# Kernel tuning notes

Measured on AMD Instinct MI355X. Metric: run time of the kernel, lower is better.

The kernel has to match this reference:

```python
import jax, jax.numpy as jnp
import numpy as np

B, N, DIM, H, DH = 8, 1024, 512, 8, 64
INNER = H * DH
SCALE = DH ** -0.5


def setup_inputs() -> dict:
    key = jax.random.key(0)
    ks = jax.random.split(key, 9)
    s = 0.02
    return {
        "x": jax.random.normal(ks[0], (B, N, DIM), jnp.float32),
        "lidar": jax.random.normal(ks[1], (B, N, INNER), jnp.float32),
        "w_qkv": jax.random.normal(ks[2], (3 * INNER, DIM), jnp.float32) * s,
        "w_merge": jax.random.normal(ks[3], (DH, DH), jnp.float32) * s,
        "b_merge": jnp.zeros((DH,), jnp.float32),
        "w_out": jax.random.normal(ks[4], (DIM, INNER), jnp.float32) * s,
        "b_out": jnp.zeros((DIM,), jnp.float32),
        "conv_w": jax.random.normal(ks[5], (2,), jnp.float32) * 0.5,
        "conv_b": jnp.zeros((), jnp.float32),
    }


def _split_heads(t):  # [b, n, h*d] -> [b, h, n, d]
    b, n, _ = t.shape
    return t.reshape(b, n, H, DH).transpose(0, 2, 1, 3)


def reference(x, lidar, w_qkv, w_merge, b_merge, w_out, b_out, conv_w, conv_b):
    b, n, _ = x.shape
    qkv = x @ w_qkv.T  # [b, n, 3*inner]
    q, k, v = jnp.split(qkv, 3, axis=-1)
    q, k, v = _split_heads(q), _split_heads(k), _split_heads(v)
    lid = _split_heads(lidar)

    dots = jnp.einsum('bhid,bhjd->bhij', q, k) * SCALE
    lidar_sim = jnp.einsum('bhid,bhjd->bhij', lid, lid) * SCALE
    lidar_sim = jax.nn.softmax(lidar_sim, axis=-1)

    # 1x1 conv over 2 channels == learned linear blend of the two score maps
    mid = conv_w[0] * dots + conv_w[1] * lidar_sim + conv_b
    attn = jax.nn.softmax(mid, axis=-1)

    out = jnp.einsum('bhij,bhjd->bhid', attn, v)
    out = out @ w_merge.T + b_merge                  # per-head linear_merge
    out = out.transpose(0, 2, 1, 3).reshape(b, n, INNER)  # b h n d -> b n (h d)
    out = out @ w_out.T + b_out                      # to_out (dropout = identity)
    return (out, lidar)
```

## Files before the change

kernel.cpp:

```cpp
#include <hip/hip_runtime.h>
#include <hip/hip_bf16.h>

#define B_      8
#define N_      1024
#define DIM_    512
#define H_      8
#define DH_     64
#define INNER_  512
#define SCALE_  0.125f
#define LOG2E_  1.4426950408889634f

typedef __attribute__((ext_vector_type(8))) __bf16         bf16x8;
typedef __attribute__((ext_vector_type(8))) unsigned short ushort8;
typedef __attribute__((ext_vector_type(4))) float          f32x4;

union FragCast { ushort8 u; bf16x8 b; };
union FragU32  { unsigned int u[4]; bf16x8 b; };

__device__ inline bf16x8 ld_frag(const unsigned short* p) {
    FragCast f; f.u = *(const ushort8*)p; return f.b;
}

__device__ inline f32x4 mfma16(bf16x8 a, bf16x8 b, f32x4 c) {
    return __builtin_amdgcn_mfma_f32_16x16x32_bf16(a, b, c, 0, 0, 0);
}

__device__ inline float fexp2(float x) { return __builtin_amdgcn_exp2f(x); }

__device__ inline unsigned short f2bf(float x) {
    unsigned int u = __float_as_uint(x);
    unsigned int lsb = (u >> 16) & 1u;
    u += 0x7fffu + lsb;
    return (unsigned short)(u >> 16);
}

__device__ inline unsigned int pack_bf2(float hi, float lo) {
    return __builtin_amdgcn_perm(__float_as_uint(hi), __float_as_uint(lo), 0x07060302u);
}

__device__ inline void gl_lds(const unsigned short* g, unsigned short* l) {
    __builtin_amdgcn_global_load_lds(
        (const __attribute__((address_space(1))) unsigned int*)g,
        (__attribute__((address_space(3))) unsigned int*)l, 16, 0, 0);
}

__global__ __launch_bounds__(256) void k_convert(
    const float* __restrict__ x, const float* __restrict__ lidar,
    const float* __restrict__ wqkv, const float* __restrict__ wmerge,
    const float* __restrict__ wout,
    unsigned short* __restrict__ x_bf, unsigned short* __restrict__ lid_bf,
    float* __restrict__ out_lidar,
    unsigned short* __restrict__ wqkv_bf, unsigned short* __restrict__ wm_bf,
    unsigned short* __restrict__ wout_bf)
{
    const int bx = blockIdx.x, tid = threadIdx.x;
    const float* src; unsigned short* dst; bool isLid = false; long base;
    if (bx < 1024)      { src = x;      dst = x_bf;    base = (long)bx * 1024; }
    else if (bx < 2048) { src = lidar;  dst = lid_bf;  base = (long)(bx - 1024) * 1024; isLid = true; }
    else if (bx < 2240) { src = wqkv;   dst = wqkv_bf; base = (long)(bx - 2048) * 1024; }
    else if (bx < 2304) { src = wout;   dst = wout_bf; base = (long)(bx - 2240) * 1024; }
    else                { src = wmerge; dst = wm_bf;   base = 0; }
    for (int k = 0; k < 4; k++) {
        long j = base + k * 256 + tid;
        float4 v = ((const float4*)src)[j];
        ushort4 o;
        o.x = f2bf(v.x); o.y = f2bf(v.y); o.z = f2bf(v.z); o.w = f2bf(v.w);
        ((ushort4*)dst)[j] = o;
        if (isLid) ((float4*)out_lidar)[j] = v;
    }
}

__global__ __launch_bounds__(256) void k_gemm_qkv(
    const unsigned short* __restrict__ A, const unsigned short* __restrict__ Bm,
    unsigned short* __restrict__ C, unsigned short* __restrict__ vt,
    int M, int Nd, int K)
{
    __shared__ unsigned short sMem[128 * 136];
    unsigned short* sA = sMem;
    unsigned short* sB = sMem + 128 * 64;
    const int tid  = threadIdx.x;
    const int lane = tid & 63, wave = tid >> 6;
    const int q = lane >> 4, l15 = lane & 15, l7 = l15 & 7;
    const int xq0 = (q ^ l7) << 3, xq4 = ((q + 4) ^ l7) << 3;
    const int m0 = blockIdx.x * 128, n0 = blockIdx.y * 128;
    const int wm = (wave >> 1) * 64, wn = (wave & 1) * 64;
    f32x4 acc[4][4] = {};

    for (int k0 = 0; k0 < K; k0 += 64) {
        __syncthreads();
        for (int i = 0; i < 4; i++) {
            int c = i * 256 + tid;
            int row = c >> 3;
            int gcol = ((c & 7) ^ (row & 7)) << 3;
            gl_lds(&A[(long)(m0 + row) * K + k0 + gcol], &sA[c * 8]);
            gl_lds(&Bm[(long)(n0 + row) * K + k0 + gcol], &sB[c * 8]);
        }
        __syncthreads();
        for (int kk = 0; kk < 2; kk++) {
            const int xx = kk ? xq4 : xq0;
            bf16x8 af[4], bfr[4];
            for (int i = 0; i < 4; i++)
                af[i]  = ld_frag(&sA[(wm + i * 16 + l15) * 64 + xx]);
            for (int i = 0; i < 4; i++)
                bfr[i] = ld_frag(&sB[(wn + i * 16 + l15) * 64 + xx]);
            for (int mi = 0; mi < 4; mi++)
                for (int ni = 0; ni < 4; ni++)
                    acc[mi][ni] = mfma16(af[mi], bfr[ni], acc[mi][ni]);
        }
    }
    if (n0 < 1024) {
        for (int mi = 0; mi < 4; mi++)
            for (int ni = 0; ni < 4; ni++)
                for (int r = 0; r < 4; r++) {
                    int row = m0 + wm + mi * 16 + q * 4 + r;
                    int col = n0 + wn + ni * 16 + l15;
                    C[(long)row * Nd + col] = f2bf(acc[mi][ni][r]);
                }
    } else {
        __syncthreads();
        for (int mi = 0; mi < 4; mi++) {
            int t0 = wm + mi * 16 + q * 4;
            for (int ni = 0; ni < 4; ni++) {
                int f = wn + ni * 16 + l15;
                ushort4 o4;
                o4.x = f2bf(acc[mi][ni][0]); o4.y = f2bf(acc[mi][ni][1]);
                o4.z = f2bf(acc[mi][ni][2]); o4.w = f2bf(acc[mi][ni][3]);
                *(ushort4*)&sMem[f * 136 + t0] = o4;
            }
        }
        __syncthreads();
        const long fb = (long)(n0 - 1024) * (B_ * N_) + m0;
        for (int i = 0; i < 8; i++) {
            int g = i * 256 + tid;
            int f = g >> 4, grp = g & 15;
            int base = (grp >> 2) * 32 + (grp & 3) * 4;
            ushort4 a4 = *(const ushort4*)&sMem[f * 136 + base];
            ushort4 b4 = *(const ushort4*)&sMem[f * 136 + base + 16];
            ushort8 o8 = {a4.x, a4.y, a4.z, a4.w, b4.x, b4.y, b4.z, b4.w};
            *(ushort8*)&vt[fb + (long)f * (B_ * N_) + grp * 8] = o8;
        }
    }
}

__global__ __launch_bounds__(256) void k_gemm_out(
    const unsigned short* __restrict__ A, const unsigned short* __restrict__ Bm,
    const float* __restrict__ bias, float* __restrict__ C, int M, int Nd, int K)
{
    __shared__ unsigned short sA[128 * 64];
    __shared__ unsigned short sB[64 * 64];
    const int tid  = threadIdx.x;
    const int lane = tid & 63, wave = tid >> 6;
    const int q = lane >> 4, l15 = lane & 15, l7 = l15 & 7;
    const int xq0 = (q ^ l7) << 3, xq4 = ((q + 4) ^ l7) << 3;
    const int m0 = blockIdx.x * 128, n0 = blockIdx.y * 64;
    const int wm = (wave >> 1) * 64, wn = (wave & 1) * 32;
    f32x4 acc[4][2] = {};

    for (int k0 = 0; k0 < K; k0 += 64) {
        __syncthreads();
        for (int i = 0; i < 4; i++) {
            int c = i * 256 + tid;
            int row = c >> 3;
            int gcol = ((c & 7) ^ (row & 7)) << 3;
            gl_lds(&A[(long)(m0 + row) * K + k0 + gcol], &sA[c * 8]);
            if (i < 2)
                gl_lds(&Bm[(long)(n0 + row) * K + k0 + gcol], &sB[c * 8]);
        }
        __syncthreads();
        for (int kk = 0; kk < 2; kk++) {
            const int xx = kk ? xq4 : xq0;
            bf16x8 af[4], bfr[2];
            for (int i = 0; i < 4; i++)
                af[i]  = ld_frag(&sA[(wm + i * 16 + l15) * 64 + xx]);
            for (int i = 0; i < 2; i++)
                bfr[i] = ld_frag(&sB[(wn + i * 16 + l15) * 64 + xx]);
            for (int mi = 0; mi < 4; mi++)
                for (int ni = 0; ni < 2; ni++)
                    acc[mi][ni] = mfma16(af[mi], bfr[ni], acc[mi][ni]);
        }
    }
    for (int mi = 0; mi < 4; mi++)
        for (int ni = 0; ni < 2; ni++)
            for (int r = 0; r < 4; r++) {
                int row = m0 + wm + mi * 16 + q * 4 + r;
                int col = n0 + wn + ni * 16 + l15;
                C[(long)row * Nd + col] = acc[mi][ni][r] + bias[col];
            }
}

__global__ __launch_bounds__(256) void k_flash(
    const unsigned short* __restrict__ qkv_bf, const unsigned short* __restrict__ lid_bf,
    const unsigned short* __restrict__ vt,
    const unsigned short* __restrict__ wm_bf, const float* __restrict__ b_merge,
    const float* __restrict__ conv_w, const float* __restrict__ conv_b,
    unsigned short* __restrict__ tmp_bf)
{
    __shared__ unsigned short sK[64 * 64];
    __shared__ unsigned short sLid[64 * 64];
    __shared__ unsigned short sVT[64 * 64];
    __shared__ unsigned short sO[4 * 16 * 72];
    __shared__ float sRS[4][16];

    const int tid = threadIdx.x, lane = tid & 63, wave = tid >> 6;
    const int q = lane >> 4, l15 = lane & 15, l7 = l15 & 7;
    const int xq0 = (q ^ l7) << 3, xq4 = ((q + 4) ^ l7) << 3;
    const int bh = blockIdx.x, itile = blockIdx.y;
    const int b = bh >> 3, h = bh & 7;
    const int i0w = itile * 64 + wave * 16;
    const long rowB = (long)b * N_;
    const int colh = h * DH_;
    const float k0c = conv_w[0] * SCALE_ * LOG2E_;
    const float k2c = conv_b[0] * LOG2E_;
    const float c1L = conv_w[1] * LOG2E_;
    const float sc = SCALE_ * LOG2E_;

    int c0i = tid, c1i = 256 + tid;
    int row0 = c0i >> 3, row1 = c1i >> 3;
    int gc0 = ((c0i & 7) ^ (row0 & 7)) << 3;
    int gc1 = ((c1i & 7) ^ (row1 & 7)) << 3;
    unsigned short* dK0 = &sK[c0i * 8];   unsigned short* dK1 = &sK[c1i * 8];
    unsigned short* dL0 = &sLid[c0i * 8]; unsigned short* dL1 = &sLid[c1i * 8];
    unsigned short* dV0 = &sVT[c0i * 8];  unsigned short* dV1 = &sVT[c1i * 8];
    const unsigned short* gK0 = &qkv_bf[(rowB + row0) * 1536 + 512 + colh + gc0];
    const unsigned short* gK1 = &qkv_bf[(rowB + row1) * 1536 + 512 + colh + gc1];
    const unsigned short* gL0 = &lid_bf[(rowB + row0) * INNER_ + colh + gc0];
    const unsigned short* gL1 = &lid_bf[(rowB + row1) * INNER_ + colh + gc1];
    const unsigned short* gV0 = &vt[(long)(colh + row0) * (B_ * N_) + rowB + gc0];
    const unsigned short* gV1 = &vt[(long)(colh + row1) * (B_ * N_) + rowB + gc1];

    const unsigned short *sK_r[4], *sL_r[4];
    for (int ns = 0; ns < 4; ns++) {
        sK_r[ns] = &sK[(ns * 16 + l15) * 64];
        sL_r[ns] = &sLid[(ns * 16 + l15) * 64];
    }

    bf16x8 qf[2], lfq[2];
    for (int ks = 0; ks < 2; ks++) {
        qf[ks]  = ld_frag(&qkv_bf[(rowB + i0w + l15) * 1536 + colh + ks * 32 + q * 8]);
        lfq[ks] = ld_frag(&lid_bf[(rowB + i0w + l15) * INNER_ + colh + ks * 32 + q * 8]);
    }

    float rsl = 0.f;
    {
        const unsigned short* p0 = gL0;
        const unsigned short* p1 = gL1;
        for (int j0 = 0; j0 < N_; j0 += 64) {
            __syncthreads();
            gl_lds(p0, dL0);
            gl_lds(p1, dL1);
            p0 += 64 * INNER_; p1 += 64 * INNER_;
            __syncthreads();
            for (int ns = 0; ns < 4; ns++) {
                f32x4 cv = {0.f, 0.f, 0.f, 0.f};
                cv = mfma16(ld_frag(sL_r[ns] + xq0), lfq[0], cv);
                cv = mfma16(ld_frag(sL_r[ns] + xq4), lfq[1], cv);
                for (int r = 0; r < 4; r++) rsl += fexp2(cv[r] * sc);
            }
        }
    }
    rsl += __shfl_xor(rsl, 16);
    rsl += __shfl_xor(rsl, 32);
    const float k1 = c1L / rsl;

    float rs = 0.f;
    f32x4 o[4] = {};

    for (int j0 = 0; j0 < N_; j0 += 64) {
        __syncthreads();
        gl_lds(gK0, dK0); gl_lds(gK1, dK1);
        gl_lds(gL0, dL0); gl_lds(gL1, dL1);
        gl_lds(gV0, dV0); gl_lds(gV1, dV1);
        gK0 += 64 * 1536;  gK1 += 64 * 1536;
        gL0 += 64 * INNER_; gL1 += 64 * INNER_;
        gV0 += 64;          gV1 += 64;
        __syncthreads();

        for (int ns2 = 0; ns2 < 2; ns2++) {
            FragU32 fa;
            for (int h2 = 0; h2 < 2; h2++) {
                int ns = ns2 * 2 + h2;
                f32x4 a = {0.f, 0.f, 0.f, 0.f};
                a = mfma16(ld_frag(sK_r[ns] + xq0), qf[0], a);
                a = mfma16(ld_frag(sK_r[ns] + xq4), qf[1], a);
                f32x4 cv = {0.f, 0.f, 0.f, 0.f};
                cv = mfma16(ld_frag(sL_r[ns] + xq0), lfq[0], cv);
                cv = mfma16(ld_frag(sL_r[ns] + xq4), lfq[1], cv);
                float pv[4];
                for (int r = 0; r < 4; r++) {
                    float els = fexp2(cv[r] * sc);
                    float t = fmaf(k0c, a[r], k2c);
                    t = fmaf(k1, els, t);
                    pv[r] = fexp2(t);
                    rs += pv[r];
                }
                fa.u[h2 * 2 + 0] = pack_bf2(pv[1], pv[0]);
                fa.u[h2 * 2 + 1] = pack_bf2(pv[3], pv[2]);
            }
            for (int dt = 0; dt < 4; dt++) {
                int vrow = dt * 16 + l15;
                bf16x8 vb = ld_frag(&sVT[vrow * 64 + (((ns2 * 4 + q) ^ l7) << 3)]);
                o[dt] = mfma16(fa.b, vb, o[dt]);
            }
        }
    }

    rs += __shfl_xor(rs, 16);
    rs += __shfl_xor(rs, 32);
    if (q == 0) sRS[wave][l15] = rs;
    float invr[4];
    for (int r = 0; r < 4; r++) invr[r] = 1.f / sRS[wave][q * 4 + r];

    unsigned short* pO = &sO[wave * 16 * 72];
    for (int dt = 0; dt < 4; dt++)
        for (int r = 0; r < 4; r++)
            pO[(q * 4 + r) * 72 + dt * 16 + l15] = f2bf(o[dt][r] * invr[r]);

    f32x4 mo[4] = {};
    for (int ks = 0; ks < 2; ks++) {
        bf16x8 af = ld_frag(&pO[l15 * 72 + ks * 32 + q * 8]);
        for (int ns = 0; ns < 4; ns++) {
            bf16x8 wf = ld_frag(&wm_bf[(ns * 16 + l15) * 64 + ks * 32 + q * 8]);
            mo[ns] = mfma16(af, wf, mo[ns]);
        }
    }
    for (int ns = 0; ns < 4; ns++) {
        float bm = b_merge[ns * 16 + l15];
        for (int r = 0; r < 4; r++) {
            long row = rowB + i0w + q * 4 + r;
            tmp_bf[row * INNER_ + colh + ns * 16 + l15] = f2bf(mo[ns][r] + bm);
        }
    }
}

extern "C" void kernel_launch(void* const* d_in, const int* in_sizes, int n_in,
                              void* d_out, int out_size, void* d_ws, size_t ws_size,
                              hipStream_t stream) {
    const float* x       = (const float*)d_in[0];
    const float* lidar   = (const float*)d_in[1];
    const float* w_qkv   = (const float*)d_in[2];
    const float* w_merge = (const float*)d_in[3];
    const float* b_merge = (const float*)d_in[4];
    const float* w_out   = (const float*)d_in[5];
    const float* b_out   = (const float*)d_in[6];
    const float* conv_w  = (const float*)d_in[7];
    const float* conv_b  = (const float*)d_in[8];

    float* out0      = (float*)d_out;
    float* out_lidar = out0 + (long)B_ * N_ * INNER_;

    size_t off = 0;
    auto carve = [&](size_t bytes) {
        void* p = (char*)d_ws + off;
        off += (bytes + 255) & ~(size_t)255;
        return p;
    };
    unsigned short* qkv_bf  = (unsigned short*)carve((size_t)B_ * N_ * 3 * INNER_ * 2);
    unsigned short* lid_bf  = (unsigned short*)carve((size_t)B_ * N_ * INNER_ * 2);
    unsigned short* x_bf    = (unsigned short*)carve((size_t)B_ * N_ * DIM_ * 2);
    unsigned short* wqkv_bf = (unsigned short*)carve((size_t)3 * INNER_ * DIM_ * 2);
    unsigned short* wout_bf = (unsigned short*)carve((size_t)DIM_ * INNER_ * 2);
    unsigned short* wm_bf   = (unsigned short*)carve((size_t)DH_ * DH_ * 2);
    unsigned short* tmp_bf  = (unsigned short*)carve((size_t)B_ * N_ * INNER_ * 2);
    unsigned short* vt_bf   = (unsigned short*)carve((size_t)INNER_ * B_ * N_ * 2);

    k_convert<<<2305, 256, 0, stream>>>(x, lidar, w_qkv, w_merge, w_out,
                                        x_bf, lid_bf, out_lidar,
                                        wqkv_bf, wm_bf, wout_bf);

    k_gemm_qkv<<<dim3(64, 12), 256, 0, stream>>>(
        x_bf, wqkv_bf, qkv_bf, vt_bf, B_ * N_, 3 * INNER_, DIM_);

    k_flash<<<dim3(64, 16), 256, 0, stream>>>(
        qkv_bf, lid_bf, vt_bf, wm_bf, b_merge, conv_w, conv_b, tmp_bf);

    k_gemm_out<<<dim3(64, 8), 256, 0, stream>>>(
        tmp_bf, wout_bf, b_out, out0, B_ * N_, DIM_, INNER_);
}
```

Measured before the change: 193.1 us.

## Widen flash block to 128 query rows, sharing K/lidar/V tiles across 8 waves

The attention kernel now runs 512 threads (8 waves), each block covering 128 query rows instead of 64, so every K, lidar and V^T tile staged in LDS is reused by twice as many waves. The grid is halved, and the lidar-softmax prepass loads 128-row tiles into the unified shared buffer. Shared memory is merged into one array, and the output staging reuses it after an added barrier. Loops get explicit unroll pragmas. This cuts global/L2 traffic per query row, at the cost of fewer blocks for scheduling and larger per-block barriers.

```diff
diff --git a/kernel.cpp b/kernel.cpp
--- a/kernel.cpp
+++ b/kernel.cpp
@@ -188,25 +188,25 @@
             }
 }
 
-__global__ __launch_bounds__(256) void k_flash(
+__global__ __launch_bounds__(512) void k_flash(
     const unsigned short* __restrict__ qkv_bf, const unsigned short* __restrict__ lid_bf,
     const unsigned short* __restrict__ vt,
     const unsigned short* __restrict__ wm_bf, const float* __restrict__ b_merge,
     const float* __restrict__ conv_w, const float* __restrict__ conv_b,
     unsigned short* __restrict__ tmp_bf)
 {
-    __shared__ unsigned short sK[64 * 64];
-    __shared__ unsigned short sLid[64 * 64];
-    __shared__ unsigned short sVT[64 * 64];
-    __shared__ unsigned short sO[4 * 16 * 72];
-    __shared__ float sRS[4][16];
+    __shared__ unsigned short smem[3 * 64 * 64];
+    __shared__ float sRS[8][16];
+    unsigned short* sK   = smem;
+    unsigned short* sLid = smem + 4096;
+    unsigned short* sVT  = smem + 8192;
 
     const int tid = threadIdx.x, lane = tid & 63, wave = tid >> 6;
     const int q = lane >> 4, l15 = lane & 15, l7 = l15 & 7;
     const int xq0 = (q ^ l7) << 3, xq4 = ((q + 4) ^ l7) << 3;
-    const int bh = blockIdx.x, itile = blockIdx.y;
+    const int bh = blockIdx.x, ipair = blockIdx.y;
     const int b = bh >> 3, h = bh & 7;
-    const int i0w = itile * 64 + wave * 16;
+    const int i0w = ipair * 128 + wave * 16;
     const long rowB = (long)b * N_;
     const int colh = h * DH_;
     const float k0c = conv_w[0] * SCALE_ * LOG2E_;
@@ -214,48 +214,44 @@
     const float c1L = conv_w[1] * LOG2E_;
     const float sc = SCALE_ * LOG2E_;
 
-    int c0i = tid, c1i = 256 + tid;
-    int row0 = c0i >> 3, row1 = c1i >> 3;
-    int gc0 = ((c0i & 7) ^ (row0 & 7)) << 3;
-    int gc1 = ((c1i & 7) ^ (row1 & 7)) << 3;
-    unsigned short* dK0 = &sK[c0i * 8];   unsigned short* dK1 = &sK[c1i * 8];
-    unsigned short* dL0 = &sLid[c0i * 8]; unsigned short* dL1 = &sLid[c1i * 8];
-    unsigned short* dV0 = &sVT[c0i * 8];  unsigned short* dV1 = &sVT[c1i * 8];
-    const unsigned short* gK0 = &qkv_bf[(rowB + row0) * 1536 + 512 + colh + gc0];
-    const unsigned short* gK1 = &qkv_bf[(rowB + row1) * 1536 + 512 + colh + gc1];
-    const unsigned short* gL0 = &lid_bf[(rowB + row0) * INNER_ + colh + gc0];
-    const unsigned short* gL1 = &lid_bf[(rowB + row1) * INNER_ + colh + gc1];
-    const unsigned short* gV0 = &vt[(long)(colh + row0) * (B_ * N_) + rowB + gc0];
-    const unsigned short* gV1 = &vt[(long)(colh + row1) * (B_ * N_) + rowB + gc1];
-
-    const unsigned short *sK_r[4], *sL_r[4];
-    for (int ns = 0; ns < 4; ns++) {
-        sK_r[ns] = &sK[(ns * 16 + l15) * 64];
-        sL_r[ns] = &sLid[(ns * 16 + l15) * 64];
-    }
+    const int srow = tid >> 3;
+    const int sgc  = ((tid & 7) ^ (srow & 7)) << 3;
+    unsigned short* dK = &sK[tid * 8];
+    unsigned short* dL = &sLid[tid * 8];
+    unsigned short* dV = &sVT[tid * 8];
+    const unsigned short* gK = &qkv_bf[(rowB + srow) * 1536 + 512 + colh + sgc];
+    const unsigned short* gL = &lid_bf[(rowB + srow) * INNER_ + colh + sgc];
+    const unsigned short* gV = &vt[(long)(colh + srow) * (B_ * N_) + rowB + sgc];
+
+    unsigned short* dL1a = &smem[tid * 8];
+    unsigned short* dL1b = &smem[(512 + tid) * 8];
+    const unsigned short* gL1a = &lid_bf[(rowB + srow) * INNER_ + colh + sgc];
+    const unsigned short* gL1b = &lid_bf[(rowB + 64 + srow) * INNER_ + colh + sgc];
+
+    const unsigned short* sR[8];
+#pragma unroll
+    for (int ns = 0; ns < 8; ns++) sR[ns] = &smem[(ns * 16 + l15) * 64];
 
     bf16x8 qf[2], lfq[2];
+#pragma unroll
     for (int ks = 0; ks < 2; ks++) {
         qf[ks]  = ld_frag(&qkv_bf[(rowB + i0w + l15) * 1536 + colh + ks * 32 + q * 8]);
         lfq[ks] = ld_frag(&lid_bf[(rowB + i0w + l15) * INNER_ + colh + ks * 32 + q * 8]);
     }
 
     float rsl = 0.f;
-    {
-        const unsigned short* p0 = gL0;
-        const unsigned short* p1 = gL1;
-        for (int j0 = 0; j0 < N_; j0 += 64) {
-            __syncthreads();
-            gl_lds(p0, dL0);
-            gl_lds(p1, dL1);
-            p0 += 64 * INNER_; p1 += 64 * INNER_;
-            __syncthreads();
-            for (int ns = 0; ns < 4; ns++) {
-                f32x4 cv = {0.f, 0.f, 0.f, 0.f};
-                cv = mfma16(ld_frag(sL_r[ns] + xq0), lfq[0], cv);
-                cv = mfma16(ld_frag(sL_r[ns] + xq4), lfq[1], cv);
-                for (int r = 0; r < 4; r++) rsl += fexp2(cv[r] * sc);
-            }
+    for (int j0 = 0; j0 < N_; j0 += 128) {
+        __syncthreads();
+        gl_lds(gL1a, dL1a);
+        gl_lds(gL1b, dL1b);
+        gL1a += 128 * INNER_; gL1b += 128 * INNER_;
+        __syncthreads();
+#pragma unroll
+        for (int ns = 0; ns < 8; ns++) {
+            f32x4 cv = {0.f, 0.f, 0.f, 0.f};
+            cv = mfma16(ld_frag(sR[ns] + xq0), lfq[0], cv);
+            cv = mfma16(ld_frag(sR[ns] + xq4), lfq[1], cv);
+            for (int r = 0; r < 4; r++) rsl += fexp2(cv[r] * sc);
         }
     }
     rsl += __shfl_xor(rsl, 16);
@@ -267,24 +263,22 @@
 
     for (int j0 = 0; j0 < N_; j0 += 64) {
         __syncthreads();
-        gl_lds(gK0, dK0); gl_lds(gK1, dK1);
-        gl_lds(gL0, dL0); gl_lds(gL1, dL1);
-        gl_lds(gV0, dV0); gl_lds(gV1, dV1);
-        gK0 += 64 * 1536;  gK1 += 64 * 1536;
-        gL0 += 64 * INNER_; gL1 += 64 * INNER_;
-        gV0 += 64;          gV1 += 64;
-        __syncthreads();
-
+        gl_lds(gK, dK); gl_lds(gL, dL); gl_lds(gV, dV);
+        gK += 64 * 1536; gL += 64 * INNER_; gV += 64;
+        __syncthreads();
+
+#pragma unroll
         for (int ns2 = 0; ns2 < 2; ns2++) {
             FragU32 fa;
+#pragma unroll
             for (int h2 = 0; h2 < 2; h2++) {
                 int ns = ns2 * 2 + h2;
                 f32x4 a = {0.f, 0.f, 0.f, 0.f};
-                a = mfma16(ld_frag(sK_r[ns] + xq0), qf[0], a);
-                a = mfma16(ld_frag(sK_r[ns] + xq4), qf[1], a);
+                a = mfma16(ld_frag(sR[ns] + xq0), qf[0], a);
+                a = mfma16(ld_frag(sR[ns] + xq4), qf[1], a);
                 f32x4 cv = {0.f, 0.f, 0.f, 0.f};
-                cv = mfma16(ld_frag(sL_r[ns] + xq0), lfq[0], cv);
-                cv = mfma16(ld_frag(sL_r[ns] + xq4), lfq[1], cv);
+                cv = mfma16(ld_frag(sR[ns + 4] + xq0), lfq[0], cv);
+                cv = mfma16(ld_frag(sR[ns + 4] + xq4), lfq[1], cv);
                 float pv[4];
                 for (int r = 0; r < 4; r++) {
                     float els = fexp2(cv[r] * sc);
@@ -296,6 +290,7 @@
                 fa.u[h2 * 2 + 0] = pack_bf2(pv[1], pv[0]);
                 fa.u[h2 * 2 + 1] = pack_bf2(pv[3], pv[2]);
             }
+#pragma unroll
             for (int dt = 0; dt < 4; dt++) {
                 int vrow = dt * 16 + l15;
                 bf16x8 vb = ld_frag(&sVT[vrow * 64 + (((ns2 * 4 + q) ^ l7) << 3)]);
@@ -310,19 +305,24 @@
     float invr[4];
     for (int r = 0; r < 4; r++) invr[r] = 1.f / sRS[wave][q * 4 + r];
 
-    unsigned short* pO = &sO[wave * 16 * 72];
+    __syncthreads();
+    unsigned short* pO = &smem[wave * 16 * 72];
+#pragma unroll
     for (int dt = 0; dt < 4; dt++)
         for (int r = 0; r < 4; r++)
             pO[(q * 4 + r) * 72 + dt * 16 + l15] = f2bf(o[dt][r] * invr[r]);
 
     f32x4 mo[4] = {};
+#pragma unroll
     for (int ks = 0; ks < 2; ks++) {
         bf16x8 af = ld_frag(&pO[l15 * 72 + ks * 32 + q * 8]);
+#pragma unroll
         for (int ns = 0; ns < 4; ns++) {
             bf16x8 wf = ld_frag(&wm_bf[(ns * 16 + l15) * 64 + ks * 32 + q * 8]);
             mo[ns] = mfma16(af, wf, mo[ns]);
         }
     }
+#pragma unroll
     for (int ns = 0; ns < 4; ns++) {
         float bm = b_merge[ns * 16 + l15];
         for (int r = 0; r < 4; r++) {
@@ -370,7 +370,7 @@
     k_gemm_qkv<<<dim3(64, 12), 256, 0, stream>>>(
         x_bf, wqkv_bf, qkv_bf, vt_bf, B_ * N_, 3 * INNER_, DIM_);
 
-    k_flash<<<dim3(64, 16), 256, 0, stream>>>(
+    k_flash<<<dim3(64, 8), 512, 0, stream>>>(
         qkv_bf, lid_bf, vt_bf, wm_bf, b_merge, conv_w, conv_b, tmp_bf);
 
     k_gemm_out<<<dim3(64, 8), 256, 0, stream>>>(
```

Measured after the change: 179.0 us. -7.3%, faster.
